# Kernel tuning notes

Measured on AMD Instinct MI355X. Metric: run time of the kernel, lower is better.

The kernel has to match this reference:

```python
import jax, jax.numpy as jnp
import numpy as np

BLOCK = 32  # GGML quantization block size (Q4_0 style)
Q_OFFSET = 8.0  # 4-bit values stored unsigned in [0,16), centered by -8


def setup_inputs() -> dict:
    key = jax.random.key(0)
    k1, k2, k3, k4, k5, k6 = jax.random.split(key, 6)
    O, I, R, T = 4096, 4096, 16, 8192
    x = jax.random.normal(k1, (T, I), dtype=jnp.float32)
    qweight = jax.random.randint(k2, (O, I), 0, 16, dtype=jnp.int32)
    scales = jax.random.uniform(k3, (O, I // BLOCK), dtype=jnp.float32)
    lora_a = jax.random.normal(k4, (O, R), dtype=jnp.float32)
    lora_b = jax.random.normal(k5, (R, I), dtype=jnp.float32)
    bias = jax.random.normal(k6, (O,), dtype=jnp.float32)
    return {"x": x, "qweight": qweight, "scales": scales,
            "lora_a": lora_a, "lora_b": lora_b, "bias": bias}


def reference(x, qweight, scales, lora_a, lora_b, bias):
    # --- dequantize_tensor: per-block scale * centered int codes ---
    O, I = qweight.shape
    q = qweight.astype(jnp.float32) - Q_OFFSET            # [O, I]
    w = (q.reshape(O, I // BLOCK, BLOCK) * scales[:, :, None]).reshape(O, I)
    # --- patch application (LoRA-style additive patch) ---
    w = w + lora_a @ lora_b                               # [O, I]
    # --- downstream consumption: linear layer ---
    y = x @ w.T + bias                                    # [T, O]
    return y
```

## Files before the change

### kernel.cpp

```cpp
#include <hip/hip_runtime.h>
#include <hip/hip_bf16.h>

typedef unsigned short u16;
typedef __attribute__((ext_vector_type(4))) float f32x4;
typedef __attribute__((ext_vector_type(8))) short bf16x8;
typedef __attribute__((ext_vector_type(8))) u16 u16x8;

#define GLDS16(g, l) __builtin_amdgcn_global_load_lds( \
    (const __attribute__((address_space(1))) void*)(g), \
    (__attribute__((address_space(3))) void*)(l), 16, 0, 0)

__device__ inline u16 f2bf(float f) {
  union { float f; unsigned u; } v; v.f = f;
  unsigned r = v.u + 0x7fffu + ((v.u >> 16) & 1u);
  return (u16)(r >> 16);
}

__global__ __launch_bounds__(256) void k_dequant_lora(
    const int* __restrict__ qw, const float* __restrict__ sc,
    const float* __restrict__ la, const float* __restrict__ lb,
    u16* __restrict__ W)
{
  const int I = 4096, R = 16;
  __shared__ float lbs[16][512];
  __shared__ float las[256];
  const int c0 = blockIdx.x * 512;
  const int o0 = blockIdx.y * 16;
  const int tid = threadIdx.x;

  las[tid] = la[(size_t)(o0 + (tid >> 4)) * R + (tid & 15)];
  #pragma unroll
  for (int i = 0; i < 8; ++i) {
    int idx = tid + i * 256;
    int r = idx >> 7;
    int cc4 = (idx & 127) << 2;
    *(float4*)&lbs[r][cc4] = *(const float4*)&lb[(size_t)r * I + c0 + cc4];
  }
  __syncthreads();

  const int cc = (tid & 63) * 8;
  const int rg = tid >> 6;
  #pragma unroll
  for (int rr = 0; rr < 4; ++rr) {
    const int o = o0 + rg * 4 + rr;
    float acc[8] = {0.f,0.f,0.f,0.f,0.f,0.f,0.f,0.f};
    #pragma unroll
    for (int r = 0; r < 16; ++r) {
      float av = las[(rg * 4 + rr) * 16 + r];
      float4 b0 = *(const float4*)&lbs[r][cc];
      float4 b1 = *(const float4*)&lbs[r][cc + 4];
      acc[0] += av * b0.x; acc[1] += av * b0.y;
      acc[2] += av * b0.z; acc[3] += av * b0.w;
      acc[4] += av * b1.x; acc[5] += av * b1.y;
      acc[6] += av * b1.z; acc[7] += av * b1.w;
    }
    const int4* qp = (const int4*)&qw[(size_t)o * I + c0 + cc];
    int4 q0 = qp[0], q1 = qp[1];
    float s = sc[(size_t)o * (I / 32) + ((c0 + cc) >> 5)];
    u16x8 w;
    w[0] = f2bf(((float)q0.x - 8.0f) * s + acc[0]);
    w[1] = f2bf(((float)q0.y - 8.0f) * s + acc[1]);
    w[2] = f2bf(((float)q0.z - 8.0f) * s + acc[2]);
    w[3] = f2bf(((float)q0.w - 8.0f) * s + acc[3]);
    w[4] = f2bf(((float)q1.x - 8.0f) * s + acc[4]);
    w[5] = f2bf(((float)q1.y - 8.0f) * s + acc[5]);
    w[6] = f2bf(((float)q1.z - 8.0f) * s + acc[6]);
    w[7] = f2bf(((float)q1.w - 8.0f) * s + acc[7]);
    *(u16x8*)&W[(size_t)o * I + c0 + cc] = w;
  }
}

__global__ __launch_bounds__(256) void k_cvt(const float* __restrict__ x,
                                             u16* __restrict__ xb)
{
  const size_t n = (size_t)8192 * 4096;
  const size_t stride = (size_t)gridDim.x * 256 * 8;
  for (size_t i = ((size_t)blockIdx.x * 256 + threadIdx.x) * 8; i < n; i += stride) {
    float4 a = *(const float4*)&x[i];
    float4 b = *(const float4*)&x[i + 4];
    u16x8 o;
    o[0] = f2bf(a.x); o[1] = f2bf(a.y); o[2] = f2bf(a.z); o[3] = f2bf(a.w);
    o[4] = f2bf(b.x); o[5] = f2bf(b.y); o[6] = f2bf(b.z); o[7] = f2bf(b.w);
    *(u16x8*)&xb[i] = o;
  }
}

__global__ __launch_bounds__(256) void k_gemm(
    const u16* __restrict__ A, const u16* __restrict__ B,
    const float* __restrict__ bias, float* __restrict__ C)
{
  const int M = 8192, N = 4096, K = 4096;
  (void)M;
  __shared__ u16 As[128 * 32];
  __shared__ u16 Bs[128 * 32];

  const int nwg = gridDim.x;
  const int cpx = nwg >> 3;
  const int bid = blockIdx.x;
  const int swz = (bid & 7) * cpx + (bid >> 3);
  const int ntn = N / 128;
  const int m0 = (swz / ntn) * 128;
  const int n0 = (swz % ntn) * 128;

  const int tid = threadIdx.x;
  const int wave = tid >> 6, lane = tid & 63;
  const int wm = (wave >> 1) * 64, wn = (wave & 1) * 64;
  const int fr = lane & 15;
  const int fk = (lane >> 4) * 8;

  const int srow0 = wave * 16 + (lane >> 2);
  const int scol = (lane & 3) * 8;
  const u16* Ag0 = A + (size_t)(m0 + srow0) * K + scol;
  const u16* Ag1 = Ag0 + (size_t)64 * K;
  const u16* Bg0 = B + (size_t)(n0 + srow0) * K + scol;
  const u16* Bg1 = Bg0 + (size_t)64 * K;
  u16* Asd0 = &As[(size_t)wave * 512];
  u16* Asd1 = &As[(size_t)(4 + wave) * 512];
  u16* Bsd0 = &Bs[(size_t)wave * 512];
  u16* Bsd1 = &Bs[(size_t)(4 + wave) * 512];

  f32x4 acc[4][4] = {};

  for (int k0 = 0; k0 < K; k0 += 32) {
    __syncthreads();
    GLDS16(Ag0 + k0, Asd0);
    GLDS16(Ag1 + k0, Asd1);
    GLDS16(Bg0 + k0, Bsd0);
    GLDS16(Bg1 + k0, Bsd1);
    __syncthreads();

    bf16x8 a[4], b[4];
    #pragma unroll
    for (int m = 0; m < 4; ++m)
      a[m] = *(const bf16x8*)&As[(wm + m * 16 + fr) * 32 + fk];
    #pragma unroll
    for (int n = 0; n < 4; ++n)
      b[n] = *(const bf16x8*)&Bs[(wn + n * 16 + fr) * 32 + fk];
    #pragma unroll
    for (int m = 0; m < 4; ++m)
      #pragma unroll
      for (int n = 0; n < 4; ++n)
        acc[m][n] = __builtin_amdgcn_mfma_f32_16x16x32_bf16(a[m], b[n], acc[m][n], 0, 0, 0);
  }

  const int crow = m0 + wm + (lane >> 4) * 4;
  const int ccol = n0 + wn + fr;
  #pragma unroll
  for (int n = 0; n < 4; ++n) {
    float bv = bias[ccol + n * 16];
    #pragma unroll
    for (int m = 0; m < 4; ++m) {
      #pragma unroll
      for (int j = 0; j < 4; ++j) {
        C[(size_t)(crow + m * 16 + j) * N + ccol + n * 16] = acc[m][n][j] + bv;
      }
    }
  }
}

extern "C" void kernel_launch(void* const* d_in, const int* in_sizes, int n_in,
                              void* d_out, int out_size, void* d_ws, size_t ws_size,
                              hipStream_t stream) {
  const float* x    = (const float*)d_in[0];
  const int*   qw   = (const int*)d_in[1];
  const float* sc   = (const float*)d_in[2];
  const float* la   = (const float*)d_in[3];
  const float* lb   = (const float*)d_in[4];
  const float* bias = (const float*)d_in[5];
  float* y = (float*)d_out;

  u16* W  = (u16*)d_ws;
  u16* Xb = (u16*)((char*)d_ws + (size_t)32 * 1024 * 1024);

  dim3 gridD(4096 / 512, 4096 / 16);
  k_dequant_lora<<<gridD, 256, 0, stream>>>(qw, sc, la, lb, W);
  k_cvt<<<2048, 256, 0, stream>>>(x, Xb);
  const int ngemm = (8192 / 128) * (4096 / 128);
  k_gemm<<<ngemm, 256, 0, stream>>>(Xb, W, bias, y);
}
```

Before: 435.0 us.

## Rewrite GEMM with 256x256 tiles, 8 waves, 4-stage LDS pipeline and swizzle

Rewrites the bf16 GEMM to use 256x256 output tiles with 512 threads (8 waves, each computing 128x64). Global-to-LDS loads now run through a 4-buffer ring, prefetched two K-steps ahead and split across two half-iterations with explicit waitcnt and barriers. An XOR swizzle on the LDS layout is meant to avoid bank conflicts, and s_setprio is raised around the MFMA blocks. The aim is to hide memory latency and raise arithmetic intensity, at the cost of more LDS (128KB) and registers per block, which limits occupancy to the two blocks requested by launch_bounds.

```diff
diff --git a/kernel.cpp b/kernel.cpp
--- a/kernel.cpp
+++ b/kernel.cpp
@@ -85,71 +85,106 @@
   }
 }
 
-__global__ __launch_bounds__(256) void k_gemm(
+__global__ __launch_bounds__(512, 2) void k_gemm(
     const u16* __restrict__ A, const u16* __restrict__ B,
     const float* __restrict__ bias, float* __restrict__ C)
 {
-  const int M = 8192, N = 4096, K = 4096;
-  (void)M;
-  __shared__ u16 As[128 * 32];
-  __shared__ u16 Bs[128 * 32];
-
-  const int nwg = gridDim.x;
-  const int cpx = nwg >> 3;
+  const int N = 4096, K = 4096;
+  const int NTK = 128;
+  __shared__ u16 As[4 * 8192];
+  __shared__ u16 Bs[4 * 8192];
+
   const int bid = blockIdx.x;
-  const int swz = (bid & 7) * cpx + (bid >> 3);
-  const int ntn = N / 128;
-  const int m0 = (swz / ntn) * 128;
-  const int n0 = (swz % ntn) * 128;
+  const int swz = (bid & 7) * 64 + (bid >> 3);
+  const int m0 = (swz >> 4) * 256;
+  const int n0 = (swz & 15) * 256;
 
   const int tid = threadIdx.x;
-  const int wave = tid >> 6, lane = tid & 63;
-  const int wm = (wave >> 1) * 64, wn = (wave & 1) * 64;
-  const int fr = lane & 15;
-  const int fk = (lane >> 4) * 8;
-
-  const int srow0 = wave * 16 + (lane >> 2);
-  const int scol = (lane & 3) * 8;
-  const u16* Ag0 = A + (size_t)(m0 + srow0) * K + scol;
-  const u16* Ag1 = Ag0 + (size_t)64 * K;
-  const u16* Bg0 = B + (size_t)(n0 + srow0) * K + scol;
-  const u16* Bg1 = Bg0 + (size_t)64 * K;
-  u16* Asd0 = &As[(size_t)wave * 512];
-  u16* Asd1 = &As[(size_t)(4 + wave) * 512];
-  u16* Bsd0 = &Bs[(size_t)wave * 512];
-  u16* Bsd1 = &Bs[(size_t)(4 + wave) * 512];
-
-  f32x4 acc[4][4] = {};
-
-  for (int k0 = 0; k0 < K; k0 += 32) {
-    __syncthreads();
-    GLDS16(Ag0 + k0, Asd0);
-    GLDS16(Ag1 + k0, Asd1);
-    GLDS16(Bg0 + k0, Bsd0);
-    GLDS16(Bg1 + k0, Bsd1);
-    __syncthreads();
-
-    bf16x8 a[4], b[4];
-    #pragma unroll
-    for (int m = 0; m < 4; ++m)
-      a[m] = *(const bf16x8*)&As[(wm + m * 16 + fr) * 32 + fk];
+  const int wid = tid >> 6, lane = tid & 63;
+  const int wid_m = wid >> 2, wid_n = wid & 3;
+
+  const int st0 = wid;
+  const int st1 = 8 + wid;
+  const int srow = lane >> 2;
+  const int schunk = (((lane & 3) ^ (((lane >> 5) & 1) << 1))) * 8;
+  const u16* Asrc0 = A + (size_t)(m0 + st0 * 16 + srow) * K + schunk;
+  const u16* Asrc1 = A + (size_t)(m0 + st1 * 16 + srow) * K + schunk;
+  const u16* Bsrc0 = B + (size_t)(n0 + st0 * 16 + srow) * K + schunk;
+  const u16* Bsrc1 = B + (size_t)(n0 + st1 * 16 + srow) * K + schunk;
+
+  #define STAGE_A(buf, t) do { \
+    GLDS16(Asrc0 + (size_t)(t) * 32, &As[(buf) * 8192 + st0 * 512]); \
+    GLDS16(Asrc1 + (size_t)(t) * 32, &As[(buf) * 8192 + st1 * 512]); } while (0)
+  #define STAGE_B(buf, t) do { \
+    GLDS16(Bsrc0 + (size_t)(t) * 32, &Bs[(buf) * 8192 + st0 * 512]); \
+    GLDS16(Bsrc1 + (size_t)(t) * 32, &Bs[(buf) * 8192 + st1 * 512]); } while (0)
+
+  const int LA = (lane & 15) * 32 + (((lane >> 4) * 8) ^ ((lane & 8) ? 16 : 0));
+  const int wmb = wid_m * 8;
+  const int wnb = wid_n * 4;
+
+  f32x4 acc[8][4] = {};
+
+  STAGE_A(0, 0); STAGE_B(0, 0);
+  STAGE_A(1, 1); STAGE_B(1, 1);
+  asm volatile("s_waitcnt vmcnt(4)" ::: "memory");
+  __builtin_amdgcn_s_barrier();
+
+  for (int t = 0; t < NTK; ++t) {
+    const int b = t & 3;
+    const u16* Ab = &As[b * 8192];
+    const u16* Bb = &Bs[b * 8192];
+
+    bf16x8 af[4], bfr[4];
+    #pragma unroll
+    for (int m = 0; m < 4; ++m)
+      af[m] = *(const bf16x8*)&Ab[(wmb + m) * 512 + LA];
     #pragma unroll
     for (int n = 0; n < 4; ++n)
-      b[n] = *(const bf16x8*)&Bs[(wn + n * 16 + fr) * 32 + fk];
+      bfr[n] = *(const bf16x8*)&Bb[(wnb + n) * 512 + LA];
+    if (t + 2 < NTK) STAGE_A((t + 2) & 3, t + 2);
+    __builtin_amdgcn_s_barrier();
+    asm volatile("s_waitcnt lgkmcnt(0)" ::: "memory");
+    __builtin_amdgcn_s_setprio(1);
     #pragma unroll
     for (int m = 0; m < 4; ++m)
       #pragma unroll
       for (int n = 0; n < 4; ++n)
-        acc[m][n] = __builtin_amdgcn_mfma_f32_16x16x32_bf16(a[m], b[n], acc[m][n], 0, 0, 0);
-  }
-
-  const int crow = m0 + wm + (lane >> 4) * 4;
-  const int ccol = n0 + wn + fr;
+        acc[m][n] = __builtin_amdgcn_mfma_f32_16x16x32_bf16(af[m], bfr[n], acc[m][n], 0, 0, 0);
+    __builtin_amdgcn_s_setprio(0);
+    __builtin_amdgcn_s_barrier();
+
+    bf16x8 af2[4];
+    #pragma unroll
+    for (int m = 0; m < 4; ++m)
+      af2[m] = *(const bf16x8*)&Ab[(wmb + 4 + m) * 512 + LA];
+    if (t + 2 < NTK) {
+      STAGE_B((t + 2) & 3, t + 2);
+      asm volatile("s_waitcnt vmcnt(4)" ::: "memory");
+    } else {
+      asm volatile("s_waitcnt vmcnt(0)" ::: "memory");
+    }
+    __builtin_amdgcn_s_barrier();
+    asm volatile("s_waitcnt lgkmcnt(0)" ::: "memory");
+    __builtin_amdgcn_s_setprio(1);
+    #pragma unroll
+    for (int m = 0; m < 4; ++m)
+      #pragma unroll
+      for (int n = 0; n < 4; ++n)
+        acc[4 + m][n] = __builtin_amdgcn_mfma_f32_16x16x32_bf16(af2[m], bfr[n], acc[4 + m][n], 0, 0, 0);
+    __builtin_amdgcn_s_setprio(0);
+    __builtin_amdgcn_s_barrier();
+  }
+  #undef STAGE_A
+  #undef STAGE_B
+
+  const int crow = m0 + wid_m * 128 + ((lane >> 4) << 2);
+  const int ccol = n0 + wid_n * 64 + (lane & 15);
   #pragma unroll
   for (int n = 0; n < 4; ++n) {
     float bv = bias[ccol + n * 16];
     #pragma unroll
-    for (int m = 0; m < 4; ++m) {
+    for (int m = 0; m < 8; ++m) {
       #pragma unroll
       for (int j = 0; j < 4; ++j) {
         C[(size_t)(crow + m * 16 + j) * N + ccol + n * 16] = acc[m][n][j] + bv;
@@ -175,6 +210,6 @@
   dim3 gridD(4096 / 512, 4096 / 16);
   k_dequant_lora<<<gridD, 256, 0, stream>>>(qw, sc, la, lb, W);
   k_cvt<<<2048, 256, 0, stream>>>(x, Xb);
-  const int ngemm = (8192 / 128) * (4096 / 128);
-  k_gemm<<<ngemm, 256, 0, stream>>>(Xb, W, bias, y);
-}
+  const int ngemm = (8192 / 256) * (4096 / 256);
+  k_gemm<<<ngemm, 512, 0, stream>>>(Xb, W, bias, y);
+}
```

Measured after the change: 372.0 us. -14.5%, faster.
